# Performance work log

Hardware: AMD Instinct MI355X
Metric: run time of the kernel (lower is better)

## Reference

```python
import jax, jax.numpy as jnp
import numpy as np

E = 512   # embed_dim
H = 8     # num_heads
D = E // H  # head_dim


def setup_inputs() -> dict:
    key = jax.random.key(0)
    ks = jax.random.split(key, 13)
    B, Nq, Nk = 4, 2048, 2048
    query = jax.random.normal(ks[0], (B, Nq, E), dtype=jnp.float32)
    key_t = jax.random.normal(ks[1], (B, Nk, E), dtype=jnp.float32)
    value = jax.random.normal(ks[2], (B, Nk, E), dtype=jnp.float32)
    geometry_mask = jax.random.bernoulli(ks[3], 0.5, (B, Nq, Nk))  # True = keep
    s = 1.0 / np.sqrt(E)
    Wq = jax.random.normal(ks[4], (E, E), dtype=jnp.float32) * s
    bq = jax.random.normal(ks[5], (E,), dtype=jnp.float32) * 0.01
    Wk = jax.random.normal(ks[6], (E, E), dtype=jnp.float32) * s
    bk = jax.random.normal(ks[7], (E,), dtype=jnp.float32) * 0.01
    Wv = jax.random.normal(ks[8], (E, E), dtype=jnp.float32) * s
    bv = jax.random.normal(ks[9], (E,), dtype=jnp.float32) * 0.01
    Wo = jax.random.normal(ks[10], (E, E), dtype=jnp.float32) * s
    bo = jax.random.normal(ks[11], (E,), dtype=jnp.float32) * 0.01
    return {"query": query, "key": key_t, "value": value,
            "geometry_mask": geometry_mask,
            "Wq": Wq, "bq": bq, "Wk": Wk, "bk": bk,
            "Wv": Wv, "bv": bv, "Wo": Wo, "bo": bo}


def reference(query, key, value, geometry_mask, Wq, bq, Wk, bk, Wv, bv, Wo, bo):
    B, Nq, _ = query.shape
    Nk = key.shape[1]
    scale = D ** -0.5
    # projections -> (B, H, N, D)
    Q = (query @ Wq + bq).reshape(B, Nq, H, D).transpose(0, 2, 1, 3)
    K = (key @ Wk + bk).reshape(B, Nk, H, D).transpose(0, 2, 1, 3)
    V = (value @ Wv + bv).reshape(B, Nk, H, D).transpose(0, 2, 1, 3)
    scores = jnp.einsum('bhqd,bhkd->bhqk', Q, K) * scale
    mask = geometry_mask[:, None, :, :]  # (B,1,Nq,Nk), True = keep
    scores = jnp.where(mask, scores, -jnp.inf)
    attn = jax.nn.softmax(scores, axis=-1)  # dropout p=0 (eval)
    out = jnp.einsum('bhqk,bhkd->bhqd', attn, V)
    out = out.transpose(0, 2, 1, 3).reshape(B, Nq, E)
    return out @ Wo + bo
```

## Files before the change

kernel.cpp:

```cpp
#include <hip/hip_runtime.h>
#include <stdint.h>


typedef __attribute__((ext_vector_type(8))) short bf16x8;
typedef __attribute__((ext_vector_type(4))) float f32x4;

#define SCLQ 0.18033688011112042f

static __device__ __forceinline__ unsigned short f2bf(float f) {
    union { float f; unsigned u; } x; x.f = f;
    unsigned r = x.u + 0x7fffu + ((x.u >> 16) & 1u);
    return (unsigned short)(r >> 16);
}

static __device__ __forceinline__ f32x4 mfma16(bf16x8 a, bf16x8 b, f32x4 c) {
    return __builtin_amdgcn_mfma_f32_16x16x32_bf16(a, b, c, 0, 0, 0);
}

#define GLOAD_LDS16(g, l)                                                            \
    __builtin_amdgcn_global_load_lds((const __attribute__((address_space(1))) void*)(g), \
                                     (__attribute__((address_space(3))) void*)(l), 16, 0, 0)


__global__ __launch_bounds__(256) void cvt_x_kernel(
    const float* __restrict__ xq, const float* __restrict__ xk, const float* __restrict__ xv,
    short* __restrict__ oq, short* __restrict__ ok, short* __restrict__ ov)
{
    const float* src = (blockIdx.y == 0) ? xq : (blockIdx.y == 1) ? xk : xv;
    short* dst = (blockIdx.y == 0) ? oq : (blockIdx.y == 1) ? ok : ov;
    size_t i = (size_t)blockIdx.x * 256 + threadIdx.x;
    float4 v = ((const float4*)src)[i];
    short4 o;
    o.x = (short)f2bf(v.x); o.y = (short)f2bf(v.y);
    o.z = (short)f2bf(v.z); o.w = (short)f2bf(v.w);
    ((short4*)dst)[i] = o;
}

__global__ __launch_bounds__(256) void cvt_wt_kernel(
    const float* __restrict__ Wq, const float* __restrict__ Wk,
    const float* __restrict__ Wv, const float* __restrict__ Wo,
    short* __restrict__ WqT, short* __restrict__ WkT,
    short* __restrict__ WvT, short* __restrict__ WoT)
{
    int z = blockIdx.y;
    const float* W = (z == 0) ? Wq : (z == 1) ? Wk : (z == 2) ? Wv : Wo;
    short* WT = (z == 0) ? WqT : (z == 1) ? WkT : (z == 2) ? WvT : WoT;
    int t = blockIdx.x * 256 + threadIdx.x;
    int n = t & 511;
    int k0 = (t >> 9) * 8;
    union { short s[8]; int4 v; } u;
#pragma unroll
    for (int j = 0; j < 8; ++j) u.s[j] = (short)f2bf(W[(size_t)(k0 + j) * 512 + n]);
    *(int4*)(WT + (size_t)n * 512 + k0) = u.v;
}

__global__ __launch_bounds__(256) void pack_mask_kernel(
    const int* __restrict__ mask, unsigned long long* __restrict__ mp)
{
    int lane = threadIdx.x & 63;
    int row = blockIdx.x * 4 + (threadIdx.x >> 6);
    const int* mrow = mask + (size_t)row * 2048;
#pragma unroll 4
    for (int w = 0; w < 32; ++w) {
        unsigned long long bits = __ballot(mrow[w * 64 + lane] != 0);
        if (lane == 0) mp[(size_t)row * 32 + w] = bits;
    }
}

static __device__ __forceinline__ void gemm_body(
    const short* __restrict__ A, const short* __restrict__ BT,
    const float* __restrict__ bias, void* __restrict__ Cout, int mode,
    char* lds, int bx, int by)
{
    const int tid = threadIdx.x;
    const int lane = tid & 63;
    const int wid = tid >> 6;
    const int l15 = lane & 15, l4 = lane >> 4;
    const int m0 = by * 128;
    const int n0 = bx * 128;
    const int wr = wid >> 1, wc = wid & 1;

    f32x4 zero = {0.f, 0.f, 0.f, 0.f};
    f32x4 acc[4][4];
#pragma unroll
    for (int i = 0; i < 4; ++i)
#pragma unroll
        for (int j = 0; j < 4; ++j) acc[i][j] = zero;

    char* Alds = lds;
    char* Blds = lds + 16384;

    for (int t = 0; t < 8; ++t) {
        const int k0 = t * 64;
#pragma unroll
        for (int s = 0; s < 4; ++s) {
            int p = s * 256 + tid;
            int r = p >> 3, c = p & 7;
            GLOAD_LDS16(A + (size_t)(m0 + r) * 512 + k0 + 8 * (c ^ (r & 7)),
                        Alds + s * 4096 + wid * 1024);
            GLOAD_LDS16(BT + (size_t)(n0 + r) * 512 + k0 + 8 * (c ^ (r & 7)),
                        Blds + s * 4096 + wid * 1024);
        }
        __syncthreads();
#pragma unroll
        for (int ks = 0; ks < 2; ++ks) {
            bf16x8 af[4], bfr[4];
#pragma unroll
            for (int mb = 0; mb < 4; ++mb) {
                int row = wr * 64 + mb * 16 + l15;
                af[mb] = *(const bf16x8*)(Alds + row * 128 +
                                          ((ks * 64 + l4 * 16) ^ ((row & 7) << 4)));
            }
#pragma unroll
            for (int nb = 0; nb < 4; ++nb) {
                int row = wc * 64 + nb * 16 + l15;
                bfr[nb] = *(const bf16x8*)(Blds + row * 128 +
                                           ((ks * 64 + l4 * 16) ^ ((row & 7) << 4)));
            }
#pragma unroll
            for (int mb = 0; mb < 4; ++mb)
#pragma unroll
                for (int nb = 0; nb < 4; ++nb)
                    acc[mb][nb] = mfma16(af[mb], bfr[nb], acc[mb][nb]);
        }
        __syncthreads();
    }

#pragma unroll
    for (int nb = 0; nb < 4; ++nb) {
        int n = n0 + wc * 64 + nb * 16 + l15;
        float bv = bias[n];
#pragma unroll
        for (int mb = 0; mb < 4; ++mb) {
#pragma unroll
            for (int r = 0; r < 4; ++r) {
                int m = m0 + wr * 64 + mb * 16 + l4 * 4 + r;
                float val = acc[mb][nb][r] + bv;
                if (mode == 0) val *= SCLQ;
                if (mode == 3) {
                    ((float*)Cout)[(size_t)m * 512 + n] = val;
                } else {
                    int b = m >> 11, tok = m & 2047;
                    int h = n >> 6, d = n & 63;
                    short* o = (short*)Cout;
                    if (mode == 2)
                        o[((size_t)(b * 8 + h) * 64 + d) * 2048 + tok] = (short)f2bf(val);
                    else
                        o[((size_t)(b * 8 + h) * 2048 + tok) * 64 + d] = (short)f2bf(val);
                }
            }
        }
    }
}

__global__ __launch_bounds__(256) void gemm_qkv_kernel(
    const short* __restrict__ Xq, const short* __restrict__ Xk, const short* __restrict__ Xv,
    const short* __restrict__ WqT, const short* __restrict__ WkT, const short* __restrict__ WvT,
    const float* __restrict__ bq, const float* __restrict__ bk, const float* __restrict__ bv,
    short* __restrict__ Qw, short* __restrict__ Kw, short* __restrict__ VTw)
{
    __shared__ char lds[32768];
    int z = blockIdx.z;
    const short* A = (z == 0) ? Xq : (z == 1) ? Xk : Xv;
    const short* BT = (z == 0) ? WqT : (z == 1) ? WkT : WvT;
    const float* bias = (z == 0) ? bq : (z == 1) ? bk : bv;
    void* Cout = (z == 0) ? (void*)Qw : (z == 1) ? (void*)Kw : (void*)VTw;
    gemm_body(A, BT, bias, Cout, z, lds, blockIdx.x, blockIdx.y);
}

__global__ __launch_bounds__(256) void gemm_kernel(
    const short* __restrict__ A, const short* __restrict__ BT,
    const float* __restrict__ bias, void* __restrict__ Cout, int mode)
{
    __shared__ char lds[32768];
    gemm_body(A, BT, bias, Cout, mode, lds, blockIdx.x, blockIdx.y);
}

__global__ __launch_bounds__(512) void attn_kernel(
    const short* __restrict__ Q, const short* __restrict__ K,
    const short* __restrict__ VT, const unsigned long long* __restrict__ mp,
    short* __restrict__ AO)
{
    __shared__ char lds[65536];
    const int tid = threadIdx.x;
    const int lane = tid & 63;
    const int wid = tid >> 6;
    const int l15 = lane & 15, l4 = lane >> 4;
    const int lid = blockIdx.x;
    const int xcd = lid & 7, jj = lid >> 3;
    const int bhi = (xcd << 2) | (jj >> 4);
    const int b = bhi >> 3, h = bhi & 7;
    const int q0 = (jj & 15) * 128 + wid * 16;
    const short* Qp = Q + ((size_t)bhi * 2048 + q0) * 64;
    const short* Kp = K + (size_t)bhi * 2048 * 64;
    const short* Vp = VT + (size_t)bhi * 64 * 2048;

    const int krow = tid >> 3;
    const int kgo  = 8 * ((tid & 7) ^ (krow & 7));
    const int vrow0 = tid >> 4;
    const int vgo   = 8 * ((tid & 15) ^ (vrow0 & 7));
    const int vrow1 = 32 + vrow0;
    const int swl = l15 & 7;

#define STAGE(KT, BUF)                                                               \
    {                                                                                \
        const short* Kn = Kp + (size_t)(KT) * 128 * 64;                              \
        char* Kd = lds + (BUF) * 16384;                                              \
        GLOAD_LDS16(Kn + (size_t)krow * 64 + kgo, Kd + wid * 1024);                  \
        GLOAD_LDS16(Kn + (size_t)(64 + krow) * 64 + kgo, Kd + 8192 + wid * 1024);    \
        const short* Vn = Vp + (KT) * 128;                                           \
        char* Vd = lds + 32768 + (BUF) * 16384;                                      \
        GLOAD_LDS16(Vn + (size_t)vrow0 * 2048 + vgo, Vd + wid * 1024);               \
        GLOAD_LDS16(Vn + (size_t)vrow1 * 2048 + vgo, Vd + 8192 + wid * 1024);        \
    }

    bf16x8 qb[2];
#pragma unroll
    for (int dc = 0; dc < 2; ++dc)
        qb[dc] = *(const bf16x8*)(Qp + l15 * 64 + dc * 32 + l4 * 8);

    f32x4 o[4];
#pragma unroll
    for (int dt = 0; dt < 4; ++dt) o[dt] = f32x4{0.f, 0.f, 0.f, 0.f};
    float mrun = 0.f, lrun = 0.f;

    const unsigned long long* mr0 = mp + ((size_t)b * 2048 + q0 + l15) * 32;

    STAGE(0, 0)
    ulonglong2 mwv = *(const ulonglong2*)(mr0);
    __syncthreads();

#define HALF(H, MW)                                                                  \
    {                                                                                \
        bf16x8 ka[4][2];                                                             \
        _Pragma("unroll") for (int tb = 0; tb < 4; ++tb)                             \
            _Pragma("unroll") for (int dc = 0; dc < 2; ++dc)                         \
                ka[tb][dc] = *(const bf16x8*)(Kc + (H) * 8192 +                      \
                                              (tb * 16 + l15) * 128 +                \
                                              16 * ((dc * 4 + l4) ^ swl));           \
        bf16x8 vb[4][2];                                                             \
        _Pragma("unroll") for (int dt = 0; dt < 4; ++dt)                             \
            _Pragma("unroll") for (int kb = 0; kb < 2; ++kb) {                       \
                const char* vr = Vc + (dt * 16 + l15) * 256;                         \
                uint2 x = *(const uint2*)(vr +                                       \
                    16 * (((H) * 8 + kb * 4 + (l4 >> 1)) ^ swl) + (l4 & 1) * 8);     \
                uint2 y = *(const uint2*)(vr +                                       \
                    16 * (((H) * 8 + kb * 4 + 2 + (l4 >> 1)) ^ swl) + (l4 & 1) * 8); \
                uint4 t; t.x = x.x; t.y = x.y; t.z = y.x; t.w = y.y;                 \
                vb[dt][kb] = *(bf16x8*)&t;                                           \
            }                                                                        \
        const float nm = -mrun;                                                      \
        unsigned long long u64 = (MW) >> (l4 * 4);                                   \
        unsigned ulo = (unsigned)u64, uhi = (unsigned)(u64 >> 32);                   \
        f32x4 sv[4];                                                                 \
        _Pragma("unroll") for (int tb = 0; tb < 4; ++tb) {                           \
            unsigned us = (tb & 2) ? uhi : ulo;                                      \
            f32x4 i0;                                                                \
            _Pragma("unroll") for (int r = 0; r < 4; ++r)                            \
                i0[r] = (us & (1u << (((tb & 1) << 4) + r))) ? nm : -1e30f;          \
            sv[tb] = mfma16(ka[tb][1], qb[1], mfma16(ka[tb][0], qb[0], i0));         \
        }                                                                            \
        float pml;                                                                   \
        {                                                                            \
            f32x4 m0v;                                                               \
            _Pragma("unroll") for (int r = 0; r < 4; ++r)                            \
                m0v[r] = fmaxf(fmaxf(sv[0][r], sv[1][r]), fmaxf(sv[2][r], sv[3][r]));\
            pml = fmaxf(fmaxf(m0v[0], m0v[1]), fmaxf(m0v[2], m0v[3]));               \
        }                                                                            \
        if (__any(pml > 8.f)) {                                                      \
            float pm = fmaxf(pml, __shfl_xor(pml, 16, 64));                          \
            pm = fmaxf(pm, __shfl_xor(pm, 32, 64));                                  \
            float dm = fmaxf(pm, 0.f);                                               \
            float al = exp2f(-dm);                                                   \
            mrun += dm;                                                              \
            lrun *= al;                                                              \
            _Pragma("unroll") for (int r = 0; r < 4; ++r) {                          \
                float alr = __shfl(al, l4 * 4 + r, 64);                              \
                _Pragma("unroll") for (int dt = 0; dt < 4; ++dt) o[dt][r] *= alr;    \
            }                                                                        \
            _Pragma("unroll") for (int tb = 0; tb < 4; ++tb)                         \
                _Pragma("unroll") for (int r = 0; r < 4; ++r) sv[tb][r] -= dm;       \
        }                                                                            \
        _Pragma("unroll") for (int tb = 0; tb < 4; ++tb)                             \
            _Pragma("unroll") for (int r = 0; r < 4; ++r)                            \
                sv[tb][r] = exp2f(sv[tb][r]);                                        \
        {                                                                            \
            f32x4 t0 = (sv[0] + sv[1]) + (sv[2] + sv[3]);                            \
            lrun += (t0[0] + t0[1]) + (t0[2] + t0[3]);                               \
        }                                                                            \
        bf16x8 pa[2];                                                                \
        {                                                                            \
            uint4 t_;                                                                \
            asm("v_cvt_pk_bf16_f32 %0, %1, %2" : "=v"(t_.x) : "v"(sv[0][0]), "v"(sv[0][1])); \
            asm("v_cvt_pk_bf16_f32 %0, %1, %2" : "=v"(t_.y) : "v"(sv[0][2]), "v"(sv[0][3])); \
            asm("v_cvt_pk_bf16_f32 %0, %1, %2" : "=v"(t_.z) : "v"(sv[1][0]), "v"(sv[1][1])); \
            asm("v_cvt_pk_bf16_f32 %0, %1, %2" : "=v"(t_.w) : "v"(sv[1][2]), "v"(sv[1][3])); \
            pa[0] = *(bf16x8*)&t_;                                                   \
            asm("v_cvt_pk_bf16_f32 %0, %1, %2" : "=v"(t_.x) : "v"(sv[2][0]), "v"(sv[2][1])); \
            asm("v_cvt_pk_bf16_f32 %0, %1, %2" : "=v"(t_.y) : "v"(sv[2][2]), "v"(sv[2][3])); \
            asm("v_cvt_pk_bf16_f32 %0, %1, %2" : "=v"(t_.z) : "v"(sv[3][0]), "v"(sv[3][1])); \
            asm("v_cvt_pk_bf16_f32 %0, %1, %2" : "=v"(t_.w) : "v"(sv[3][2]), "v"(sv[3][3])); \
            pa[1] = *(bf16x8*)&t_;                                                   \
        }                                                                            \
        _Pragma("unroll") for (int dt = 0; dt < 4; ++dt)                             \
            o[dt] = mfma16(pa[1], vb[dt][1], mfma16(pa[0], vb[dt][0], o[dt]));       \
    }

    for (int kt = 0; kt < 16; ++kt) {
        const int cur = kt & 1;
        char* Kc = lds + cur * 16384;
        char* Vc = lds + 32768 + cur * 16384;
        if (kt < 15) STAGE(kt + 1, cur ^ 1)
        ulonglong2 mwn;
        mwn.x = 0; mwn.y = 0;
        if (kt < 15) mwn = *(const ulonglong2*)(mr0 + 2 * kt + 2);
        HALF(0, mwv.x)
        HALF(1, mwv.y)
        mwv = mwn;
        __syncthreads();
    }
#undef HALF
#undef STAGE

    {
        float lt = lrun;
        lt += __shfl_xor(lt, 16, 64);
        lt += __shfl_xor(lt, 32, 64);
        float inv = 1.0f / lt;
#pragma unroll
        for (int r = 0; r < 4; ++r) {
            float invr = __shfl(inv, l4 * 4 + r, 64);
            size_t base = ((size_t)b * 2048 + q0 + l4 * 4 + r) * 512 + h * 64;
#pragma unroll
            for (int dt = 0; dt < 4; ++dt)
                AO[base + dt * 16 + l15] = (short)f2bf(o[dt][r] * invr);
        }
    }
}

extern "C" void kernel_launch(void* const* d_in, const int* in_sizes, int n_in,
                              void* d_out, int out_size, void* d_ws, size_t ws_size,
                              hipStream_t stream) {
    const float* q  = (const float*)d_in[0];
    const float* k  = (const float*)d_in[1];
    const float* v  = (const float*)d_in[2];
    const int*   gm = (const int*)d_in[3];
    const float* Wq = (const float*)d_in[4];  const float* bq = (const float*)d_in[5];
    const float* Wk = (const float*)d_in[6];  const float* bk = (const float*)d_in[7];
    const float* Wv = (const float*)d_in[8];  const float* bv = (const float*)d_in[9];
    const float* Wo = (const float*)d_in[10]; const float* bo = (const float*)d_in[11];

    char* ws = (char*)d_ws;
    short* Xq  = (short*)(ws + 0);
    short* Xk  = (short*)(ws + 8388608);
    short* Xv  = (short*)(ws + 16777216);
    short* WqT = (short*)(ws + 25165824);
    short* WkT = (short*)(ws + 25690112);
    short* WvT = (short*)(ws + 26214400);
    short* WoT = (short*)(ws + 26738688);
    short* Qw  = (short*)(ws + 27262976);
    short* Kw  = (short*)(ws + 35651584);
    short* VTw = (short*)(ws + 44040192);
    short* AO  = (short*)(ws + 52428800);
    unsigned long long* MP = (unsigned long long*)(ws + 60817408);

    cvt_x_kernel<<<dim3(4096, 3), 256, 0, stream>>>(q, k, v, Xq, Xk, Xv);
    cvt_wt_kernel<<<dim3(128, 4), 256, 0, stream>>>(Wq, Wk, Wv, Wo, WqT, WkT, WvT, WoT);
    pack_mask_kernel<<<dim3(2048), 256, 0, stream>>>(gm, MP);

    gemm_qkv_kernel<<<dim3(4, 64, 3), 256, 0, stream>>>(Xq, Xk, Xv, WqT, WkT, WvT,
                                                        bq, bk, bv, Qw, Kw, VTw);

    attn_kernel<<<dim3(512), 512, 0, stream>>>(Qw, Kw, VTw, MP, AO);

    gemm_kernel<<<dim3(4, 64), 256, 0, stream>>>(AO, WoT, bo, (void*)d_out, 3);
}
```

Baseline: 165.9 us.

## Merge prep kernels and unroll attention loop with precomputed LDS addresses

Combines the three preprocessing kernels (activation cast, weight transpose-cast, mask bit-packing) into one launch that dispatches on block index, removing two launch gaps. In the attention kernel, the K/V tile loop is unrolled by two so buffer offsets become compile-time constants, and per-lane LDS read addresses are precomputed once outside the loop. It also raises wave priority around the MFMA sections with s_setprio. The larger unrolled body may raise register pressure.

```diff
diff --git a/kernel.cpp b/kernel.cpp
--- a/kernel.cpp
+++ b/kernel.cpp
@@ -21,49 +21,49 @@
     __builtin_amdgcn_global_load_lds((const __attribute__((address_space(1))) void*)(g), \
                                      (__attribute__((address_space(3))) void*)(l), 16, 0, 0)
 
-
-__global__ __launch_bounds__(256) void cvt_x_kernel(
-    const float* __restrict__ xq, const float* __restrict__ xk, const float* __restrict__ xv,
-    short* __restrict__ oq, short* __restrict__ ok, short* __restrict__ ov)
-{
-    const float* src = (blockIdx.y == 0) ? xq : (blockIdx.y == 1) ? xk : xv;
-    short* dst = (blockIdx.y == 0) ? oq : (blockIdx.y == 1) ? ok : ov;
-    size_t i = (size_t)blockIdx.x * 256 + threadIdx.x;
-    float4 v = ((const float4*)src)[i];
-    short4 o;
-    o.x = (short)f2bf(v.x); o.y = (short)f2bf(v.y);
-    o.z = (short)f2bf(v.z); o.w = (short)f2bf(v.w);
-    ((short4*)dst)[i] = o;
-}
-
-__global__ __launch_bounds__(256) void cvt_wt_kernel(
+__global__ __launch_bounds__(256) void prep_kernel(
+    const float* __restrict__ q, const float* __restrict__ k, const float* __restrict__ v,
+    const int* __restrict__ gm,
     const float* __restrict__ Wq, const float* __restrict__ Wk,
     const float* __restrict__ Wv, const float* __restrict__ Wo,
+    short* __restrict__ Xq, short* __restrict__ Xk, short* __restrict__ Xv,
     short* __restrict__ WqT, short* __restrict__ WkT,
-    short* __restrict__ WvT, short* __restrict__ WoT)
-{
-    int z = blockIdx.y;
-    const float* W = (z == 0) ? Wq : (z == 1) ? Wk : (z == 2) ? Wv : Wo;
-    short* WT = (z == 0) ? WqT : (z == 1) ? WkT : (z == 2) ? WvT : WoT;
-    int t = blockIdx.x * 256 + threadIdx.x;
-    int n = t & 511;
-    int k0 = (t >> 9) * 8;
-    union { short s[8]; int4 v; } u;
-#pragma unroll
-    for (int j = 0; j < 8; ++j) u.s[j] = (short)f2bf(W[(size_t)(k0 + j) * 512 + n]);
-    *(int4*)(WT + (size_t)n * 512 + k0) = u.v;
-}
-
-__global__ __launch_bounds__(256) void pack_mask_kernel(
-    const int* __restrict__ mask, unsigned long long* __restrict__ mp)
-{
-    int lane = threadIdx.x & 63;
-    int row = blockIdx.x * 4 + (threadIdx.x >> 6);
-    const int* mrow = mask + (size_t)row * 2048;
+    short* __restrict__ WvT, short* __restrict__ WoT,
+    unsigned long long* __restrict__ mp)
+{
+    int bx = blockIdx.x;
+    if (bx < 12288) {
+        int z = bx >> 12;
+        const float* src = (z == 0) ? q : (z == 1) ? k : v;
+        short* dst = (z == 0) ? Xq : (z == 1) ? Xk : Xv;
+        size_t i = (size_t)(bx & 4095) * 256 + threadIdx.x;
+        float4 vv = ((const float4*)src)[i];
+        short4 o;
+        o.x = (short)f2bf(vv.x); o.y = (short)f2bf(vv.y);
+        o.z = (short)f2bf(vv.z); o.w = (short)f2bf(vv.w);
+        ((short4*)dst)[i] = o;
+    } else if (bx < 12800) {
+        int b2 = bx - 12288;
+        int z = b2 >> 7;
+        const float* W = (z == 0) ? Wq : (z == 1) ? Wk : (z == 2) ? Wv : Wo;
+        short* WT = (z == 0) ? WqT : (z == 1) ? WkT : (z == 2) ? WvT : WoT;
+        int t = (b2 & 127) * 256 + threadIdx.x;
+        int n = t & 511;
+        int k0 = (t >> 9) * 8;
+        union { short s[8]; int4 v4; } u;
+#pragma unroll
+        for (int j = 0; j < 8; ++j) u.s[j] = (short)f2bf(W[(size_t)(k0 + j) * 512 + n]);
+        *(int4*)(WT + (size_t)n * 512 + k0) = u.v4;
+    } else {
+        int b3 = bx - 12800;
+        int lane = threadIdx.x & 63;
+        int row = b3 * 4 + (threadIdx.x >> 6);
+        const int* mrow = gm + (size_t)row * 2048;
 #pragma unroll 4
-    for (int w = 0; w < 32; ++w) {
-        unsigned long long bits = __ballot(mrow[w * 64 + lane] != 0);
-        if (lane == 0) mp[(size_t)row * 32 + w] = bits;
+        for (int w = 0; w < 32; ++w) {
+            unsigned long long bits = __ballot(mrow[w * 64 + lane] != 0);
+            if (lane == 0) mp[(size_t)row * 32 + w] = bits;
+        }
     }
 }
 
@@ -214,6 +214,15 @@
         GLOAD_LDS16(Vn + (size_t)vrow1 * 2048 + vgo, Vd + 8192 + wid * 1024);        \
     }
 
+    const int lh = l4 >> 1;
+    const char* pK0 = lds + l15 * 128 + 16 * (l4 ^ swl);
+    const char* pK1 = lds + l15 * 128 + 16 * ((4 + l4) ^ swl);
+    const char* bV = lds + 32768 + l15 * 256 + (l4 & 1) * 8;
+    const char* pVx0 = bV + 16 * (lh ^ swl);
+    const char* pVy0 = bV + 16 * ((2 + lh) ^ swl);
+    const char* pVx1 = bV + 16 * ((4 + lh) ^ swl);
+    const char* pVy1 = bV + 16 * ((6 + lh) ^ swl);
+
     bf16x8 qb[2];
 #pragma unroll
     for (int dc = 0; dc < 2; ++dc)
@@ -226,33 +235,29 @@
 
     const unsigned long long* mr0 = mp + ((size_t)b * 2048 + q0 + l15) * 32;
 
-    STAGE(0, 0)
-    ulonglong2 mwv = *(const ulonglong2*)(mr0);
-    __syncthreads();
-
-#define HALF(H, MW)                                                                  \
+#define BODY(H, CUR, MW)                                                             \
     {                                                                                \
         bf16x8 ka[4][2];                                                             \
-        _Pragma("unroll") for (int tb = 0; tb < 4; ++tb)                             \
-            _Pragma("unroll") for (int dc = 0; dc < 2; ++dc)                         \
-                ka[tb][dc] = *(const bf16x8*)(Kc + (H) * 8192 +                      \
-                                              (tb * 16 + l15) * 128 +                \
-                                              16 * ((dc * 4 + l4) ^ swl));           \
+        _Pragma("unroll") for (int tb = 0; tb < 4; ++tb) {                           \
+            ka[tb][0] = *(const bf16x8*)(pK0 + ((CUR) * 16384 + (H) * 8192) + tb * 2048); \
+            ka[tb][1] = *(const bf16x8*)(pK1 + ((CUR) * 16384 + (H) * 8192) + tb * 2048); \
+        }                                                                            \
         bf16x8 vb[4][2];                                                             \
-        _Pragma("unroll") for (int dt = 0; dt < 4; ++dt)                             \
-            _Pragma("unroll") for (int kb = 0; kb < 2; ++kb) {                       \
-                const char* vr = Vc + (dt * 16 + l15) * 256;                         \
-                uint2 x = *(const uint2*)(vr +                                       \
-                    16 * (((H) * 8 + kb * 4 + (l4 >> 1)) ^ swl) + (l4 & 1) * 8);     \
-                uint2 y = *(const uint2*)(vr +                                       \
-                    16 * (((H) * 8 + kb * 4 + 2 + (l4 >> 1)) ^ swl) + (l4 & 1) * 8); \
-                uint4 t; t.x = x.x; t.y = x.y; t.z = y.x; t.w = y.y;                 \
-                vb[dt][kb] = *(bf16x8*)&t;                                           \
-            }                                                                        \
+        _Pragma("unroll") for (int dt = 0; dt < 4; ++dt) {                           \
+            uint2 x0 = *(const uint2*)(pVx0 + ((CUR) * 16384 + (H) * 128) + dt * 4096); \
+            uint2 y0 = *(const uint2*)(pVy0 + ((CUR) * 16384 + (H) * 128) + dt * 4096); \
+            uint2 x1 = *(const uint2*)(pVx1 + ((CUR) * 16384 + (H) * 128) + dt * 4096); \
+            uint2 y1 = *(const uint2*)(pVy1 + ((CUR) * 16384 + (H) * 128) + dt * 4096); \
+            uint4 ta; ta.x = x0.x; ta.y = x0.y; ta.z = y0.x; ta.w = y0.y;            \
+            vb[dt][0] = *(bf16x8*)&ta;                                               \
+            uint4 tb4; tb4.x = x1.x; tb4.y = x1.y; tb4.z = y1.x; tb4.w = y1.y;       \
+            vb[dt][1] = *(bf16x8*)&tb4;                                              \
+        }                                                                            \
         const float nm = -mrun;                                                      \
         unsigned long long u64 = (MW) >> (l4 * 4);                                   \
         unsigned ulo = (unsigned)u64, uhi = (unsigned)(u64 >> 32);                   \
         f32x4 sv[4];                                                                 \
+        __builtin_amdgcn_s_setprio(1);                                               \
         _Pragma("unroll") for (int tb = 0; tb < 4; ++tb) {                           \
             unsigned us = (tb & 2) ? uhi : ulo;                                      \
             f32x4 i0;                                                                \
@@ -260,6 +265,7 @@
                 i0[r] = (us & (1u << (((tb & 1) << 4) + r))) ? nm : -1e30f;          \
             sv[tb] = mfma16(ka[tb][1], qb[1], mfma16(ka[tb][0], qb[0], i0));         \
         }                                                                            \
+        __builtin_amdgcn_s_setprio(0);                                               \
         float pml;                                                                   \
         {                                                                            \
             f32x4 m0v;                                                               \
@@ -302,24 +308,33 @@
             asm("v_cvt_pk_bf16_f32 %0, %1, %2" : "=v"(t_.w) : "v"(sv[3][2]), "v"(sv[3][3])); \
             pa[1] = *(bf16x8*)&t_;                                                   \
         }                                                                            \
+        __builtin_amdgcn_s_setprio(1);                                               \
         _Pragma("unroll") for (int dt = 0; dt < 4; ++dt)                             \
             o[dt] = mfma16(pa[1], vb[dt][1], mfma16(pa[0], vb[dt][0], o[dt]));       \
-    }
-
-    for (int kt = 0; kt < 16; ++kt) {
-        const int cur = kt & 1;
-        char* Kc = lds + cur * 16384;
-        char* Vc = lds + 32768 + cur * 16384;
-        if (kt < 15) STAGE(kt + 1, cur ^ 1)
-        ulonglong2 mwn;
-        mwn.x = 0; mwn.y = 0;
-        if (kt < 15) mwn = *(const ulonglong2*)(mr0 + 2 * kt + 2);
-        HALF(0, mwv.x)
-        HALF(1, mwv.y)
+        __builtin_amdgcn_s_setprio(0);                                               \
+    }
+
+    STAGE(0, 0)
+    ulonglong2 mwv = *(const ulonglong2*)(mr0);
+    __syncthreads();
+
+    for (int kt2 = 0; kt2 < 8; ++kt2) {
+        STAGE(2 * kt2 + 1, 1)
+        ulonglong2 mwn = *(const ulonglong2*)(mr0 + 4 * kt2 + 2);
+        BODY(0, 0, mwv.x)
+        BODY(1, 0, mwv.y)
         mwv = mwn;
         __syncthreads();
-    }
-#undef HALF
+        if (kt2 < 7) {
+            STAGE(2 * kt2 + 2, 0)
+            mwn = *(const ulonglong2*)(mr0 + 4 * kt2 + 4);
+        }
+        BODY(0, 1, mwv.x)
+        BODY(1, 1, mwv.y)
+        mwv = mwn;
+        __syncthreads();
+    }
+#undef BODY
 #undef STAGE
 
     {
@@ -364,9 +379,8 @@
     short* AO  = (short*)(ws + 52428800);
     unsigned long long* MP = (unsigned long long*)(ws + 60817408);
 
-    cvt_x_kernel<<<dim3(4096, 3), 256, 0, stream>>>(q, k, v, Xq, Xk, Xv);
-    cvt_wt_kernel<<<dim3(128, 4), 256, 0, stream>>>(Wq, Wk, Wv, Wo, WqT, WkT, WvT, WoT);
-    pack_mask_kernel<<<dim3(2048), 256, 0, stream>>>(gm, MP);
+    prep_kernel<<<dim3(14848), 256, 0, stream>>>(q, k, v, gm, Wq, Wk, Wv, Wo,
+                                                 Xq, Xk, Xv, WqT, WkT, WvT, WoT, MP);
 
     gemm_qkv_kernel<<<dim3(4, 64, 3), 256, 0, stream>>>(Xq, Xk, Xv, WqT, WkT, WvT,
                                                         bq, bk, bv, Qw, Kw, VTw);
```

New measurement: 176.4 us. +6.4%, slower.
